# Performance work log

Measured on AMD Instinct MI355X. Metric: run time of the kernel, lower is better.

## Reference

```python
import jax, jax.numpy as jnp
import numpy as np

CH = [32, 64, 128, 256, 512]
# per decoder stage s (s=0 deepest): conv_a Cin = CH[3-s] + in_ch, Cout = CH[3-s]; conv_b CH[3-s]->CH[3-s]
STAGE_DIMS = [(768, 256), (384, 128), (192, 64), (96, 32)]


def three_interpolation(p1, p2, x2):
    """p1 [B,N1,3] dense coords, p2 [B,N2,3] sparse coords, x2 [B,C,N2] -> [B,C,N1]."""
    d2 = (jnp.sum(p1 * p1, -1)[:, :, None]
          - 2.0 * jnp.einsum('bnd,bmd->bnm', p1, p2)
          + jnp.sum(p2 * p2, -1)[:, None, :])            # [B,N1,N2] squared dists
    neg_d, idx = jax.lax.top_k(-d2, 3)                   # 3 nearest neighbors
    dist = jnp.maximum(-neg_d, 0.0)                      # [B,N1,3]
    w = 1.0 / (dist + 1e-8)
    w = w / jnp.sum(w, axis=-1, keepdims=True)           # inverse-distance weights
    gathered = jax.vmap(lambda x, i: x[:, i])(x2, idx)   # [B,C,N1,3]
    return jnp.einsum('bcnk,bnk->bcn', gathered, w)


def conv_bn_relu(x, W, g, b):
    # 1x1 conv1d + BN (eval: running mean 0, var 1) + ReLU
    y = jnp.einsum('oc,bcn->bon', W, x)
    return jax.nn.relu(y * g[None, :, None] + b[None, :, None])


def setup_inputs() -> dict:
    key = jax.random.key(0)
    B = 8
    Ns = [8192, 2048, 512, 128, 32]
    inp = {}
    keys = jax.random.split(key, 64)
    ki = 0
    for i, n in enumerate(Ns):
        inp[f'p{i}'] = jax.random.uniform(keys[ki], (B, n, 3), jnp.float32); ki += 1
        inp[f'f{i}'] = jax.random.normal(keys[ki], (B, CH[i], n), jnp.float32); ki += 1
    for s, (cin, cout) in enumerate(STAGE_DIMS):
        inp[f'w{s}a'] = jax.random.normal(keys[ki], (cout, cin), jnp.float32) * 0.05; ki += 1
        inp[f'g{s}a'] = 1.0 + 0.1 * jax.random.normal(keys[ki], (cout,), jnp.float32); ki += 1
        inp[f'b{s}a'] = 0.1 * jax.random.normal(keys[ki], (cout,), jnp.float32); ki += 1
        inp[f'w{s}b'] = jax.random.normal(keys[ki], (cout, cout), jnp.float32) * 0.05; ki += 1
        inp[f'g{s}b'] = 1.0 + 0.1 * jax.random.normal(keys[ki], (cout,), jnp.float32); ki += 1
        inp[f'b{s}b'] = 0.1 * jax.random.normal(keys[ki], (cout,), jnp.float32); ki += 1
    return inp


def reference(p0, p1, p2, p3, p4, f0, f1, f2, f3, f4,
              w0a, g0a, b0a, w0b, g0b, b0b,
              w1a, g1a, b1a, w1b, g1b, b1b,
              w2a, g2a, b2a, w2b, g2b, b2b,
              w3a, g3a, b3a, w3b, g3b, b3b):
    p = [p0, p1, p2, p3, p4]
    f = [f0, f1, f2, f3, f4]
    params = [(w0a, g0a, b0a, w0b, g0b, b0b),
              (w1a, g1a, b1a, w1b, g1b, b1b),
              (w2a, g2a, b2a, w2b, g2b, b2b),
              (w3a, g3a, b3a, w3b, g3b, b3b)]
    # decoder stage s propagates level (4-s) -> (3-s)
    for s in range(4):
        lvl = 3 - s
        interp = three_interpolation(p[lvl], p[lvl + 1], f[lvl + 1])
        x = jnp.concatenate([f[lvl], interp], axis=1)
        wa, ga, ba, wb, gb, bb = params[s]
        x = conv_bn_relu(x, wa, ga, ba)
        x = conv_bn_relu(x, wb, gb, bb)
        f[lvl] = x
    return f[0]
```

## Files before the change

### kernel.cpp

```cpp
#include <hip/hip_runtime.h>

#define KNN_INF 3.0e38f

struct PackAll {
    const float* src[4];
    float4* dst[4];
    int c1, c2, c3;
};
__global__ void pack_kernel(PackAll P, int total) {
    int t = blockIdx.x * 256 + threadIdx.x;
    if (t >= total) return;
    int s = (t >= P.c1) + (t >= P.c2) + (t >= P.c3);
    int start = (s == 0) ? 0 : (s == 1) ? P.c1 : (s == 2) ? P.c2 : P.c3;
    int i = t - start;
    const float* q = P.src[s] + (size_t)i * 3;
    float x = q[0], y = q[1], z = q[2];
    P.dst[s][i] = make_float4(x, y, z, x * x + y * y + z * z);
}

struct KnnAll4 {
    const float* p1[4];
    const float4* c4[4];
    float* pd[4]; int* pi[4];
    int N1[4], N2[4], chunk[4], nchunk[4], nbx[4];
    int bs1, bs2, bs3;
};
__global__ __launch_bounds__(256) void knn_all_kernel(KnnAll4 P) {
    int bid = blockIdx.x;
    int s = (bid >= P.bs1) + (bid >= P.bs2) + (bid >= P.bs3);
    int start = (s == 0) ? 0 : (s == 1) ? P.bs1 : (s == 2) ? P.bs2 : P.bs3;
    int local = bid - start;
    int nbx = P.nbx[s];
    int bx = local % nbx;
    int rest = local / nbx;
    int b = rest & 7;
    int z = rest >> 3;
    int N1 = P.N1[s], N2 = P.N2[s], chunk = P.chunk[s], nchunk = P.nchunk[s];
    int m0 = z * chunk;
    const float4* __restrict__ cb = P.c4[s] + (size_t)b * N2 + m0;
    int n = bx * 256 + threadIdx.x;
    if (n >= N1) return;
    const float* p1b = P.p1[s] + ((size_t)b * N1 + n) * 3;
    float px = p1b[0], py = p1b[1], pz = p1b[2];
    float s1 = px * px + py * py + pz * pz;
    float t0 = KNN_INF, t1 = KNN_INF, t2 = KNN_INF;
    int i0 = 0, i1 = 0, i2 = 0;
    for (int m = 0; m < chunk; ++m) {
        float4 q = cb[m];
        float dot = px * q.x + py * q.y + pz * q.z;
        float t = fmaf(-2.0f, dot, q.w);
        if (t < t2) {
            if (t < t1) {
                t2 = t1; i2 = i1;
                if (t < t0) { t1 = t0; i1 = i0; t0 = t; i0 = m; }
                else        { t1 = t;  i1 = m; }
            } else { t2 = t; i2 = m; }
        }
    }
    size_t base = (((size_t)b * N1 + n) * nchunk + z) * 3;
    float* pd = P.pd[s]; int* pi = P.pi[s];
    pd[base + 0] = s1 + t0; pd[base + 1] = s1 + t1; pd[base + 2] = s1 + t2;
    pi[base + 0] = m0 + i0; pi[base + 1] = m0 + i1; pi[base + 2] = m0 + i2;
}

struct MergeAll4 {
    const float* pd[4]; const int* pi[4];
    int* idx[4]; float* w[4];
    int nchunk[4];
    int ts1, ts2, ts3;
};
__global__ void knn_merge_all_kernel(MergeAll4 P, int total) {
    int t = blockIdx.x * blockDim.x + threadIdx.x;
    if (t >= total) return;
    int s = (t >= P.ts1) + (t >= P.ts2) + (t >= P.ts3);
    int start = (s == 0) ? 0 : (s == 1) ? P.ts1 : (s == 2) ? P.ts2 : P.ts3;
    int lt = t - start;
    int nchunk = P.nchunk[s];
    float d0 = KNN_INF, d1 = KNN_INF, d2 = KNN_INF;
    int i0 = 0, i1 = 0, i2 = 0;
    const float* pd = P.pd[s]; const int* pi = P.pi[s];
    size_t base = (size_t)lt * nchunk * 3;
    for (int c = 0; c < nchunk * 3; ++c) {
        float d = pd[base + c];
        int   i = pi[base + c];
        if (d < d2) {
            if (d < d1) {
                d2 = d1; i2 = i1;
                if (d < d0) { d1 = d0; i1 = i0; d0 = d; i0 = i; }
                else        { d1 = d;  i1 = i; }
            } else { d2 = d; i2 = i; }
        }
    }
    float dd0 = fmaxf(d0, 0.0f), dd1 = fmaxf(d1, 0.0f), dd2 = fmaxf(d2, 0.0f);
    float w0 = 1.0f / (dd0 + 1e-8f);
    float w1 = 1.0f / (dd1 + 1e-8f);
    float w2 = 1.0f / (dd2 + 1e-8f);
    float wsum = w0 + w1 + w2;
    w0 /= wsum; w1 /= wsum; w2 /= wsum;
    size_t ob = (size_t)lt * 3;
    P.idx[s][ob + 0] = i0; P.idx[s][ob + 1] = i1; P.idx[s][ob + 2] = i2;
    P.w[s][ob + 0] = w0; P.w[s][ob + 1] = w1; P.w[s][ob + 2] = w2;
}

#define TO 32
#define TN 64
#define BK 16
template<bool PARTIAL>
__global__ __launch_bounds__(256) void conv_a_fused_kernel(
    const float* __restrict__ f1, const float* __restrict__ x2,
    const int* __restrict__ idxS, const float* __restrict__ wS,
    const float* __restrict__ W, const float* __restrict__ g, const float* __restrict__ bv,
    float* __restrict__ Y,
    int C1, int C2, int N, int N2, int Cout, int chunk) {
    __shared__ float Ws[BK][TO];
    __shared__ float Xs[BK][TN];
    int Cin = C1 + C2;
    int zb = blockIdx.z;
    int b = zb & 7;
    int split = zb >> 3;
    int kBase = split * chunk;
    int oBase = blockIdx.y * TO;
    int nBase = blockIdx.x * TN;
    int tid = threadIdx.x;
    int tx = tid & 15;
    int ty = tid >> 4;
    int nn = tid & 63;
    int kk0 = tid >> 6;
    int n = nBase + nn;
    size_t gb = ((size_t)b * N + n) * 3;
    int j0 = idxS[gb + 0], j1 = idxS[gb + 1], j2 = idxS[gb + 2];
    float w0g = wS[gb + 0], w1g = wS[gb + 1], w2g = wS[gb + 2];
    const float* f1b = f1 + (size_t)b * C1 * N;
    const float* x2b = x2 + (size_t)b * C2 * N2;
    float acc[2][4] = {{0.f, 0.f, 0.f, 0.f}, {0.f, 0.f, 0.f, 0.f}};
    for (int k0 = kBase; k0 < kBase + chunk; k0 += BK) {
        for (int t = tid; t < TO * BK; t += 256) {
            int o = t / BK, kk = t % BK;
            Ws[kk][o] = W[(size_t)(oBase + o) * Cin + k0 + kk];
        }
#pragma unroll
        for (int i = 0; i < 4; ++i) {
            int kk = kk0 + i * 4;
            int k = k0 + kk;
            float v;
            if (k < C1) {
                v = f1b[(size_t)k * N + n];
            } else {
                const float* r = x2b + (size_t)(k - C1) * N2;
                v = r[j0] * w0g + r[j1] * w1g + r[j2] * w2g;
            }
            Xs[kk][nn] = v;
        }
        __syncthreads();
#pragma unroll
        for (int kk = 0; kk < BK; ++kk) {
            float w0 = Ws[kk][ty * 2 + 0];
            float w1 = Ws[kk][ty * 2 + 1];
            float4 xv = *reinterpret_cast<const float4*>(&Xs[kk][tx * 4]);
            acc[0][0] = fmaf(w0, xv.x, acc[0][0]);
            acc[0][1] = fmaf(w0, xv.y, acc[0][1]);
            acc[0][2] = fmaf(w0, xv.z, acc[0][2]);
            acc[0][3] = fmaf(w0, xv.w, acc[0][3]);
            acc[1][0] = fmaf(w1, xv.x, acc[1][0]);
            acc[1][1] = fmaf(w1, xv.y, acc[1][1]);
            acc[1][2] = fmaf(w1, xv.z, acc[1][2]);
            acc[1][3] = fmaf(w1, xv.w, acc[1][3]);
        }
        __syncthreads();
    }
#pragma unroll
    for (int r = 0; r < 2; ++r) {
        int o = oBase + ty * 2 + r;
        float4 st;
        if (PARTIAL) {
            st.x = acc[r][0]; st.y = acc[r][1]; st.z = acc[r][2]; st.w = acc[r][3];
            *reinterpret_cast<float4*>(&Y[((size_t)zb * Cout + o) * N + nBase + tx * 4]) = st;
        } else {
            float gg = g[o], bb = bv[o];
            st.x = fmaxf(fmaf(acc[r][0], gg, bb), 0.0f);
            st.y = fmaxf(fmaf(acc[r][1], gg, bb), 0.0f);
            st.z = fmaxf(fmaf(acc[r][2], gg, bb), 0.0f);
            st.w = fmaxf(fmaf(acc[r][3], gg, bb), 0.0f);
            *reinterpret_cast<float4*>(&Y[((size_t)b * Cout + o) * N + nBase + tx * 4]) = st;
        }
    }
}

template<bool PARTIAL>
__global__ __launch_bounds__(256) void conv_gemm_kernel(
    const float* __restrict__ X, const float* __restrict__ W,
    const float* __restrict__ g, const float* __restrict__ bv,
    float* __restrict__ Y, int Cin, int Cout, int N, int chunk) {
    __shared__ float Ws[BK][TO];
    __shared__ float Xs[BK][TN];
    int zb = blockIdx.z;
    int b = zb & 7;
    int split = zb >> 3;
    int kBase = split * chunk;
    int oBase = blockIdx.y * TO;
    int nBase = blockIdx.x * TN;
    int tid = threadIdx.x;
    int tx = tid & 15;
    int ty = tid >> 4;
    float acc[2][4] = {{0.f, 0.f, 0.f, 0.f}, {0.f, 0.f, 0.f, 0.f}};
    const float* Xb = X + (size_t)b * Cin * N;
    for (int k0 = kBase; k0 < kBase + chunk; k0 += BK) {
        for (int t = tid; t < TO * BK; t += 256) {
            int o = t / BK, kk = t % BK;
            Ws[kk][o] = W[(size_t)(oBase + o) * Cin + k0 + kk];
        }
        for (int t = tid; t < BK * TN; t += 256) {
            int kk = t / TN, nnn = t % TN;
            Xs[kk][nnn] = Xb[(size_t)(k0 + kk) * N + nBase + nnn];
        }
        __syncthreads();
#pragma unroll
        for (int kk = 0; kk < BK; ++kk) {
            float w0 = Ws[kk][ty * 2 + 0];
            float w1 = Ws[kk][ty * 2 + 1];
            float4 xv = *reinterpret_cast<const float4*>(&Xs[kk][tx * 4]);
            acc[0][0] = fmaf(w0, xv.x, acc[0][0]);
            acc[0][1] = fmaf(w0, xv.y, acc[0][1]);
            acc[0][2] = fmaf(w0, xv.z, acc[0][2]);
            acc[0][3] = fmaf(w0, xv.w, acc[0][3]);
            acc[1][0] = fmaf(w1, xv.x, acc[1][0]);
            acc[1][1] = fmaf(w1, xv.y, acc[1][1]);
            acc[1][2] = fmaf(w1, xv.z, acc[1][2]);
            acc[1][3] = fmaf(w1, xv.w, acc[1][3]);
        }
        __syncthreads();
    }
#pragma unroll
    for (int r = 0; r < 2; ++r) {
        int o = oBase + ty * 2 + r;
        float4 st;
        if (PARTIAL) {
            st.x = acc[r][0]; st.y = acc[r][1]; st.z = acc[r][2]; st.w = acc[r][3];
            *reinterpret_cast<float4*>(&Y[((size_t)zb * Cout + o) * N + nBase + tx * 4]) = st;
        } else {
            float gg = g[o], bb = bv[o];
            st.x = fmaxf(fmaf(acc[r][0], gg, bb), 0.0f);
            st.y = fmaxf(fmaf(acc[r][1], gg, bb), 0.0f);
            st.z = fmaxf(fmaf(acc[r][2], gg, bb), 0.0f);
            st.w = fmaxf(fmaf(acc[r][3], gg, bb), 0.0f);
            *reinterpret_cast<float4*>(&Y[((size_t)b * Cout + o) * N + nBase + tx * 4]) = st;
        }
    }
}

__global__ void reduce_bn_relu_kernel(const float* __restrict__ part,
                                      const float* __restrict__ g,
                                      const float* __restrict__ bv,
                                      float* __restrict__ Y,
                                      int Cout, int N, int total4, int nsplit, int stride4) {
    int t = blockIdx.x * blockDim.x + threadIdx.x;
    if (t >= total4) return;
    const float4* p4 = reinterpret_cast<const float4*>(part);
    float4 a = p4[t];
    for (int s = 1; s < nsplit; ++s) {
        float4 v = p4[t + (size_t)s * stride4];
        a.x += v.x; a.y += v.y; a.z += v.z; a.w += v.w;
    }
    int o = ((t * 4) / N) % Cout;
    float gg = g[o], bb = bv[o];
    float4 st;
    st.x = fmaxf(fmaf(a.x, gg, bb), 0.0f);
    st.y = fmaxf(fmaf(a.y, gg, bb), 0.0f);
    st.z = fmaxf(fmaf(a.z, gg, bb), 0.0f);
    st.w = fmaxf(fmaf(a.w, gg, bb), 0.0f);
    reinterpret_cast<float4*>(Y)[t] = st;
}

extern "C" void kernel_launch(void* const* d_in, const int* in_sizes, int n_in,
                              void* d_out, int out_size, void* d_ws, size_t ws_size,
                              hipStream_t stream) {
    const int B = 8;
    const int Ns[5]  = {8192, 2048, 512, 128, 32};
    const int CHs[5] = {32, 64, 128, 256, 512};

    const float* p[5];
    const float* f[5];
    for (int i = 0; i < 5; ++i) {
        p[i] = (const float*)d_in[2 * i];
        f[i] = (const float*)d_in[2 * i + 1];
    }

    int N1s[4], N2s[4], C1s[4], C2s[4];
    for (int s = 0; s < 4; ++s) {
        int lvl = 3 - s;
        N1s[s] = Ns[lvl]; N2s[s] = Ns[lvl + 1];
        C1s[s] = CHs[lvl];
        C2s[s] = (s == 0) ? CHs[4] : CHs[lvl + 1];
    }
    const int nchunks[4] = {1, 4, 8, 8};
    int chunks[4], nbxs[4];
    for (int s = 0; s < 4; ++s) {
        chunks[s] = N2s[s] / nchunks[s];
        nbxs[s] = (N1s[s] + 255) / 256;
    }

    float* ws = (float*)d_ws;
    int*   knn_idx = (int*)ws;
    float* knn_w   = ws + 262144;
    float* part_d  = ws + 524288;
    int*   part_i  = (int*)(ws + 524288 + 2018304);
    float* bufA    = ws + 524288;
    float* gpart   = ws + 524288 + 2097152;
    float* out0    = ws + 4718592;
    float* out1    = ws + 4980736;
    float* out2    = ws + 5505024;
    float4* packed = (float4*)(ws + 6553600);
    float* outs[4] = {out0, out1, out2, (float*)d_out};

    int idxOff[4], pOff[4], pkOff[4];
    {
        int a = 0, q = 0, k = 0;
        for (int s = 0; s < 4; ++s) {
            idxOff[s] = a; a += B * N1s[s] * 3;
            pOff[s] = q;  q += B * N1s[s] * nchunks[s] * 3;
            pkOff[s] = k; k += B * N2s[s];
        }
    }

    PackAll PK;
    int cum = 0, cArr[4];
    for (int s = 0; s < 4; ++s) {
        PK.src[s] = p[4 - s];
        PK.dst[s] = packed + pkOff[s];
        cArr[s] = cum;
        cum += B * N2s[s];
    }
    PK.c1 = cArr[1]; PK.c2 = cArr[2]; PK.c3 = cArr[3];
    pack_kernel<<<(cum + 255) / 256, 256, 0, stream>>>(PK, cum);

    KnnAll4 KP;
    int blk = 0, bsArr[4];
    for (int s = 0; s < 4; ++s) {
        KP.p1[s] = p[3 - s];
        KP.c4[s] = packed + pkOff[s];
        KP.pd[s] = part_d + pOff[s]; KP.pi[s] = part_i + pOff[s];
        KP.N1[s] = N1s[s]; KP.N2[s] = N2s[s];
        KP.chunk[s] = chunks[s]; KP.nchunk[s] = nchunks[s]; KP.nbx[s] = nbxs[s];
        bsArr[s] = blk;
        blk += nbxs[s] * B * nchunks[s];
    }
    KP.bs1 = bsArr[1]; KP.bs2 = bsArr[2]; KP.bs3 = bsArr[3];
    knn_all_kernel<<<blk, 256, 0, stream>>>(KP);

    MergeAll4 MP;
    int tt = 0, tsArr[4];
    for (int s = 0; s < 4; ++s) {
        MP.pd[s] = part_d + pOff[s]; MP.pi[s] = part_i + pOff[s];
        MP.idx[s] = knn_idx + idxOff[s]; MP.w[s] = knn_w + idxOff[s];
        MP.nchunk[s] = nchunks[s];
        tsArr[s] = tt;
        tt += B * N1s[s];
    }
    MP.ts1 = tsArr[1]; MP.ts2 = tsArr[2]; MP.ts3 = tsArr[3];
    knn_merge_all_kernel<<<(tt + 255) / 256, 256, 0, stream>>>(MP, tt);

    const int nsA[4] = {6, 3, 2, 1};
    const int nsB[4] = {4, 2, 1, 1};

    for (int s = 0; s < 4; ++s) {
        int N1 = N1s[s], N2 = N2s[s];
        int C1 = C1s[s], C2 = C2s[s];
        int Cin = C1 + C2, Cout = C1;
        const float* x2 = (s == 0) ? f[4] : outs[s - 1];
        const float* wa = (const float*)d_in[10 + s * 6 + 0];
        const float* ga = (const float*)d_in[10 + s * 6 + 1];
        const float* ba = (const float*)d_in[10 + s * 6 + 2];
        const float* wb = (const float*)d_in[10 + s * 6 + 3];
        const float* gb = (const float*)d_in[10 + s * 6 + 4];
        const float* bb = (const float*)d_in[10 + s * 6 + 5];
        const int* idxS = knn_idx + idxOff[s];
        const float* wSb = knn_w + idxOff[s];

        {
            int nsplit = nsA[s];
            int chunk = Cin / nsplit;
            dim3 grid(N1 / TN, Cout / TO, B * nsplit);
            if (nsplit == 1) {
                conv_a_fused_kernel<false><<<grid, 256, 0, stream>>>(
                    f[3 - s], x2, idxS, wSb, wa, ga, ba, bufA, C1, C2, N1, N2, Cout, chunk);
            } else {
                conv_a_fused_kernel<true><<<grid, 256, 0, stream>>>(
                    f[3 - s], x2, idxS, wSb, wa, ga, ba, gpart, C1, C2, N1, N2, Cout, chunk);
                int total4 = B * Cout * N1 / 4;
                reduce_bn_relu_kernel<<<(total4 + 255) / 256, 256, 0, stream>>>(
                    gpart, ga, ba, bufA, Cout, N1, total4, nsplit, total4);
            }
        }
        {
            int nsplit = nsB[s];
            int chunk = Cout / nsplit;
            dim3 grid(N1 / TN, Cout / TO, B * nsplit);
            if (nsplit == 1) {
                conv_gemm_kernel<false><<<grid, 256, 0, stream>>>(
                    bufA, wb, gb, bb, outs[s], Cout, Cout, N1, chunk);
            } else {
                conv_gemm_kernel<true><<<grid, 256, 0, stream>>>(
                    bufA, wb, gb, bb, gpart, Cout, Cout, N1, chunk);
                int total4 = B * Cout * N1 / 4;
                reduce_bn_relu_kernel<<<(total4 + 255) / 256, 256, 0, stream>>>(
                    gpart, gb, bb, outs[s], Cout, N1, total4, nsplit, total4);
            }
        }
    }
}
```

Baseline: 247.7 us.

## Split largest-stage KNN into dedicated LDS-tiled kernel with 4 queries per thread

The largest KNN stage (8192 dense points against 2048 sparse) moves out of the fused multi-stage kernel into its own kernel. In it, each block stages a 256-candidate chunk in shared memory and each thread handles four query points, so every candidate read is reused across four distance updates. The other three stages stay in a smaller fused kernel. This trades one extra launch and more registers per thread for less global memory traffic. The new kernel hardcodes a chunk size of 256 and assumes N1 is a multiple of 1024.

```diff
diff --git a/kernel.cpp b/kernel.cpp
--- a/kernel.cpp
+++ b/kernel.cpp
@@ -18,17 +18,65 @@
     P.dst[s][i] = make_float4(x, y, z, x * x + y * y + z * z);
 }
 
-struct KnnAll4 {
-    const float* p1[4];
-    const float4* c4[4];
-    float* pd[4]; int* pi[4];
-    int N1[4], N2[4], chunk[4], nchunk[4], nbx[4];
-    int bs1, bs2, bs3;
+__global__ __launch_bounds__(256) void knn_s3_kernel(
+    const float* __restrict__ p1,
+    const float4* __restrict__ c4,
+    float* __restrict__ pd, int* __restrict__ pi,
+    int N1, int N2, int nchunk) {
+    __shared__ float4 sm4[256];
+    int b = blockIdx.y;
+    int z = blockIdx.z;
+    int m0 = z * 256;
+    sm4[threadIdx.x] = c4[(size_t)b * N2 + m0 + threadIdx.x];
+    __syncthreads();
+    int nb = blockIdx.x * 1024 + threadIdx.x;
+    float px[4], py[4], pz[4], s1[4];
+    float t0[4], t1[4], t2[4];
+    int i0[4], i1[4], i2[4];
+#pragma unroll
+    for (int j = 0; j < 4; ++j) {
+        int n = nb + j * 256;
+        const float* pp = p1 + ((size_t)b * N1 + n) * 3;
+        px[j] = pp[0]; py[j] = pp[1]; pz[j] = pp[2];
+        s1[j] = px[j] * px[j] + py[j] * py[j] + pz[j] * pz[j];
+        t0[j] = KNN_INF; t1[j] = KNN_INF; t2[j] = KNN_INF;
+        i0[j] = 0; i1[j] = 0; i2[j] = 0;
+    }
+    for (int m = 0; m < 256; ++m) {
+        float4 q = sm4[m];
+#pragma unroll
+        for (int j = 0; j < 4; ++j) {
+            float dot = px[j] * q.x + py[j] * q.y + pz[j] * q.z;
+            float t = fmaf(-2.0f, dot, q.w);
+            if (t < t2[j]) {
+                if (t < t1[j]) {
+                    t2[j] = t1[j]; i2[j] = i1[j];
+                    if (t < t0[j]) { t1[j] = t0[j]; i1[j] = i0[j]; t0[j] = t; i0[j] = m; }
+                    else           { t1[j] = t;  i1[j] = m; }
+                } else { t2[j] = t; i2[j] = m; }
+            }
+        }
+    }
+#pragma unroll
+    for (int j = 0; j < 4; ++j) {
+        int n = nb + j * 256;
+        size_t base = (((size_t)b * N1 + n) * nchunk + z) * 3;
+        pd[base + 0] = s1[j] + t0[j]; pd[base + 1] = s1[j] + t1[j]; pd[base + 2] = s1[j] + t2[j];
+        pi[base + 0] = m0 + i0[j]; pi[base + 1] = m0 + i1[j]; pi[base + 2] = m0 + i2[j];
+    }
+}
+
+struct KnnAll3 {
+    const float* p1[3];
+    const float4* c4[3];
+    float* pd[3]; int* pi[3];
+    int N1[3], N2[3], chunk[3], nchunk[3], nbx[3];
+    int bs1, bs2;
 };
-__global__ __launch_bounds__(256) void knn_all_kernel(KnnAll4 P) {
+__global__ __launch_bounds__(256) void knn_small_kernel(KnnAll3 P) {
     int bid = blockIdx.x;
-    int s = (bid >= P.bs1) + (bid >= P.bs2) + (bid >= P.bs3);
-    int start = (s == 0) ? 0 : (s == 1) ? P.bs1 : (s == 2) ? P.bs2 : P.bs3;
+    int s = (bid >= P.bs1) + (bid >= P.bs2);
+    int start = (s == 0) ? 0 : (s == 1) ? P.bs1 : P.bs2;
     int local = bid - start;
     int nbx = P.nbx[s];
     int bx = local % nbx;
@@ -333,9 +381,16 @@
     PK.c1 = cArr[1]; PK.c2 = cArr[2]; PK.c3 = cArr[3];
     pack_kernel<<<(cum + 255) / 256, 256, 0, stream>>>(PK, cum);
 
-    KnnAll4 KP;
-    int blk = 0, bsArr[4];
-    for (int s = 0; s < 4; ++s) {
+    {
+        dim3 qg(N1s[3] / 1024, B, nchunks[3]);
+        knn_s3_kernel<<<qg, 256, 0, stream>>>(p[0], packed + pkOff[3],
+                                              part_d + pOff[3], part_i + pOff[3],
+                                              N1s[3], N2s[3], nchunks[3]);
+    }
+
+    KnnAll3 KP;
+    int blk = 0, bsArr[3];
+    for (int s = 0; s < 3; ++s) {
         KP.p1[s] = p[3 - s];
         KP.c4[s] = packed + pkOff[s];
         KP.pd[s] = part_d + pOff[s]; KP.pi[s] = part_i + pOff[s];
@@ -344,8 +399,8 @@
         bsArr[s] = blk;
         blk += nbxs[s] * B * nchunks[s];
     }
-    KP.bs1 = bsArr[1]; KP.bs2 = bsArr[2]; KP.bs3 = bsArr[3];
-    knn_all_kernel<<<blk, 256, 0, stream>>>(KP);
+    KP.bs1 = bsArr[1]; KP.bs2 = bsArr[2];
+    knn_small_kernel<<<blk, 256, 0, stream>>>(KP);
 
     MergeAll4 MP;
     int tt = 0, tsArr[4];
```

New measurement: 322.9 us. +30.4%, slower.
